# Optimization experiments

Measured on AMD Instinct MI355X. Metric: run time of the kernel, lower is better.

Reference implementation:

```python
import jax, jax.numpy as jnp
import numpy as np

NX, NY = 512, 512
FNUM, GNUM = 120, 120
NA = 1.35
WAVELENGTH = NX * NA / 100.0  # chosen so normalized period = 100
N_LIQUID = 1.44
M_RED = 0.25
LOW_LIGHT_THRES = 1e-3
SRC_STEEP = 8.0
RESIST_STEEP = 30.0
RESIST_INT = 0.225
DOSES = (0.98, 1.0, 1.02)
SRC_GRID = 13

X1 = NX // 2 - FNUM; X2 = NX // 2 + FNUM + 1
Y1 = NY // 2 - GNUM; Y2 = NY // 2 + GNUM + 1
_PER_X = NX / (WAVELENGTH / NA)
_PER_Y = NY / (WAVELENGTH / NA)
NORM_SPEC = _PER_X * _PER_Y
DFMDG = 1.0 / NORM_SPEC
_fm = (np.arange(X1, X2) - NX // 2) / _PER_X
_gm = (np.arange(Y1, Y2) - NY // 2) / _PER_Y
_FM, _GM = np.meshgrid(_fm, _gm)  # 'xy' indexing, shape [2*GNUM+1, 2*FNUM+1]
FM = jnp.asarray(_FM, jnp.float32)
GM = jnp.asarray(_GM, jnp.float32)


def cal_pupil(fg2):
    # obliquity factor; pupil phase is identically zero in this module
    num = 1.0 - (M_RED ** 2) * (NA ** 2) * fg2
    den = 1.0 - (NA / N_LIQUID) ** 2 * fg2
    return jnp.sqrt(jnp.sqrt(num / den))


def setup_inputs() -> dict:
    key = jax.random.key(0)
    g = np.linspace(-1.0, 1.0, SRC_GRID, dtype=np.float32)
    fxg, fyg = np.meshgrid(g, g)
    r = np.sqrt(fxg ** 2 + fyg ** 2)
    data = ((r >= 0.6) & (r <= 0.9)).astype(np.float32)  # annular source
    # sigmoid activation init: +1 where lit, -1 elsewhere (zeros, set 2 where data>0.5, sub 1)
    params = 2.0 * data - 1.0
    mask_value = jax.random.uniform(key, (NY, NX), jnp.float32)
    return {
        "mask_value": mask_value,
        "source_params": jnp.asarray(params, jnp.float32),
        "source_fx": jnp.asarray(fxg.reshape(-1), jnp.float32),
        "source_fy": jnp.asarray(fyg.reshape(-1), jnp.float32),
    }


def _forward(mask_value, source_params, source_fx, source_fy):
    # source activation + low-light pruning (masked_select expressed as zero-weighting)
    val = jax.nn.sigmoid(SRC_STEEP * source_params).reshape(-1)  # [S]
    valid = val >= LOW_LIGHT_THRES
    w = jnp.where(valid, val, 0.0)
    weight = jnp.sum(w)

    # normalization intensity (detached in the original)
    fxy2 = source_fx ** 2 + source_fy ** 2
    obl = cal_pupil(jnp.where(valid, fxy2, 0.0))
    norm_I = jax.lax.stop_gradient(
        N_LIQUID * DFMDG ** 2 * jnp.sum(w * (NORM_SPEC * obl) ** 2) / weight
    )

    # shifted pupil per source point over the mask frequency window
    F = FM[None, :, :] + source_fx[:, None, None]  # [S, Gy, Gx]
    G = GM[None, :, :] + source_fy[:, None, None]
    rho2 = F * F + G * G                            # == mask_fg2m + 2(fx*fm+fy*gm) + fxy2
    vmask = rho2 <= 1.0
    pupil = jnp.where(vmask, cal_pupil(jnp.where(vmask, rho2, 0.0)), 0.0)  # [S, Gy, Gx]

    S = w.shape[0]
    Is, Rs = [], []
    for d in DOSES:
        fv = jnp.fft.fftshift(jnp.fft.fft2(jnp.fft.ifftshift(mask_value * d)))
        win = fv[Y1:Y2, X1:X2]                      # [Gy, Gx] complex
        tempH = win[None, :, :] * pupil.astype(jnp.complex64)  # masked spectrum*pupil
        e = jnp.zeros((S, NY, NX), jnp.complex64).at[:, Y1:Y2, X1:X2].set(tempH)
        AA = jnp.fft.fftshift(jnp.fft.ifft2(e), axes=(-2, -1))
        I2 = AA.real ** 2 + AA.imag ** 2            # |AA * conj(AA)|
        intensity = jnp.einsum('s,syx->yx', w, I2) / weight / norm_I
        Is.append(intensity)
        Rs.append(jax.nn.sigmoid(RESIST_STEEP * (intensity - RESIST_INT)))
    # [2, 3, NY, NX]: [0] = aerial intensity per dose, [1] = resist image per dose
    return jnp.stack([jnp.stack(Is), jnp.stack(Rs)])


def reference(mask_value, source_params, source_fx, source_fy):
    return _forward(mask_value, source_params, source_fx, source_fy)
```

## Files before the change

### kernel.cpp

```cpp
#include <hip/hip_runtime.h>
#include <hip/hip_bf16.h>
#include <hip/hip_fp16.h>


#define SPLIT 8

static const size_t O_ACC  = 8192;
static const size_t ACC_BYTES = (size_t)SPLIT * 512 * 512 * 4;
static const size_t O_WIN  = O_ACC + ACC_BYTES;
static const size_t O_R1   = O_WIN + 464896;
static const size_t O_T2   = O_R1 + 987136;
static const size_t SLOT_BYTES = (size_t)512 * 244 * 4;

__device__ inline float2 cadd(float2 a, float2 b){ return make_float2(a.x+b.x, a.y+b.y); }
__device__ inline float2 csub(float2 a, float2 b){ return make_float2(a.x-b.x, a.y-b.y); }
__device__ inline float2 cmul(float2 a, float2 b){
  return make_float2(fmaf(a.x, b.x, -(a.y*b.y)), fmaf(a.x, b.y, a.y*b.x));
}
__device__ inline float2 twsgn(float2 t, int S) {
  return make_float2(t.x, (S > 0) ? t.y : -t.y);
}

__device__ inline void build_twt(float2* twt) {
  for (int k = (int)threadIdx.x; k < 512; k += 256) {
    double a = 6.283185307179586476925286766559 * (double)k / 512.0;
    twt[k] = make_float2((float)cos(a), (float)sin(a));
  }
}

template<int S, bool ZTOP>
__device__ inline void dft8(float2 v[8]) {
  const float sg = (float)S;
  const float C7 = 0.7071067811865476f;
  float2 t0, t1, t2, t3, t4, t5, t6, t7;
  if (ZTOP) {
    t0 = v[0]; t4 = v[0];
    t1 = v[1]; t5 = v[1];
    t2 = v[2]; t6 = v[2];
    t3 = v[3]; t7 = v[3];
  } else {
    t0=cadd(v[0],v[4]); t4=csub(v[0],v[4]);
    t1=cadd(v[1],v[5]); t5=csub(v[1],v[5]);
    t2=cadd(v[2],v[6]); t6=csub(v[2],v[6]);
    t3=cadd(v[3],v[7]); t7=csub(v[3],v[7]);
  }
  t5 = make_float2(C7*(t5.x - sg*t5.y), C7*(t5.y + sg*t5.x));
  t6 = make_float2(-sg*t6.y, sg*t6.x);
  t7 = make_float2(C7*(-t7.x - sg*t7.y), C7*(sg*t7.x - t7.y));
  float2 u0=cadd(t0,t2), u2=csub(t0,t2);
  float2 u1=cadd(t1,t3), u3=csub(t1,t3);
  u3 = make_float2(-sg*u3.y, sg*u3.x);
  float2 u4=cadd(t4,t6), u6=csub(t4,t6);
  float2 u5=cadd(t5,t7), u7=csub(t5,t7);
  u7 = make_float2(-sg*u7.y, sg*u7.x);
  v[0]=cadd(u0,u1); v[4]=csub(u0,u1);
  v[2]=cadd(u2,u3); v[6]=csub(u2,u3);
  v[1]=cadd(u4,u5); v[5]=csub(u4,u5);
  v[3]=cadd(u6,u7); v[7]=csub(u6,u7);
}

template<int S, bool ZTOP>
__device__ inline void wfft512(float2 v[8], int lane, float2* xch,
                               const float2* twt) {
  const int p2 = lane & 7, u0 = lane >> 3;
  dft8<S, ZTOP>(v);
  { float2 t1 = twsgn(twt[lane], S), acc = t1;
    v[1] = cmul(v[1], acc);
    #pragma unroll
    for (int u = 2; u < 8; u++) { acc = cmul(acc, t1); v[u] = cmul(v[u], acc); } }
  __builtin_amdgcn_wave_barrier();
  #pragma unroll
  for (int u = 0; u < 8; u++) xch[u*68 + p2*8 + u0] = v[u];
  __builtin_amdgcn_wave_barrier();
  { const float4* rp = (const float4*)(xch + u0*68 + p2*8);
    #pragma unroll
    for (int q = 0; q < 4; q++) {
      float4 t = rp[q];
      v[2*q]   = make_float2(t.x, t.y);
      v[2*q+1] = make_float2(t.z, t.w);
    } }
  dft8<S, false>(v);
  { float2 t1 = twsgn(twt[p2 << 3], S), acc = t1;
    v[1] = cmul(v[1], acc);
    #pragma unroll
    for (int u = 2; u < 8; u++) { acc = cmul(acc, t1); v[u] = cmul(v[u], acc); } }
  __builtin_amdgcn_wave_barrier();
  #pragma unroll
  for (int u = 0; u < 8; u++) xch[u*68 + lane] = v[u];
  __builtin_amdgcn_wave_barrier();
  { const float4* rp = (const float4*)(xch + p2*68 + u0*8);
    #pragma unroll
    for (int q = 0; q < 4; q++) {
      float4 t = rp[q];
      v[2*q]   = make_float2(t.x, t.y);
      v[2*q+1] = make_float2(t.z, t.w);
    } }
  dft8<S, false>(v);
}

__global__ void __launch_bounds__(256, 6) k_b1(const float* mask, const float* prm,
                                               const float* sfx, const float* sfy,
                                               char* ws, float2* R1t) {
  int t = threadIdx.x, lane = t & 63, wv = t >> 6;
  __shared__ __align__(16) float2 lds[4*544];
  __shared__ __align__(16) float2 twt[512];
  build_twt(twt);
  if (blockIdx.x == 0) {
    float*  sw  = (float*)lds;
    float*  sxx = sw + 192; float* syy = sxx + 192; float* scw = syy + 192;
    double* so  = (double*)(sw + 768);
    int*    skp = (int*)(so + 176);
    if (t < 169) {
      float p = prm[t];
      float val = 1.f / (1.f + __expf(-8.f * p));
      float w = (val >= 0.001f) ? val : 0.f;
      double o = 0.0; float fx = 0.f, fy = 0.f;
      if (w > 0.f) {
        fx = sfx[t]; fy = sfy[t];
        double f2 = (double)fx*(double)fx + (double)fy*(double)fy;
        o = (double)w * sqrt((1.0 - 0.11390625 * f2) / (1.0 - 0.87890625 * f2));
      }
      sw[t] = w; so[t] = o; sxx[t] = fx; syy[t] = fy;
    }
    __syncthreads();
    if (t < 169) {
      float w = sw[t];
      int keep = 0; float cw = w;
      if (w > 0.f) {
        float fx = sxx[t], fy = syy[t];
        int pr = -1;
        for (int s2 = 0; s2 < 169; s2++) {
          if (sw[s2] > 0.f && fabsf(sxx[s2] + fx) < 1e-5f
                           && fabsf(syy[s2] + fy) < 1e-5f) { pr = s2; break; }
        }
        if (pr < 0 || pr == t) keep = 1;
        else if (pr > t) { keep = 1; cw = w + sw[pr]; }
      }
      skp[t] = keep; scw[t] = cw;
    }
    __syncthreads();
    if (t == 0) {
      float* wsf = (float*)ws;
      double Sden = 0.0; int c = 0;
      for (int s = 0; s < 169; s++) {
        Sden += so[s];
        if (skp[s]) { wsf[64+c] = scw[s]; wsf[320+c] = sxx[s]; wsf[576+c] = syy[s]; c++; }
      }
      ((int*)ws)[0] = c;
      wsf[1] = (float)(1.0 / (262144.0 * 1.44 * Sden));
    }
  }
  __syncthreads();
  int y = blockIdx.x * 4 + wv;
  float2 v[8];
  #pragma unroll
  for (int q = 0; q < 8; q++) v[q] = make_float2(mask[y*512 + 64*q + lane], 0.f);
  wfft512<-1, false>(v, lane, lds + wv*544, twt);
  #pragma unroll
  for (int u = 0; u < 8; u++) {
    int k = (lane>>3) + 8*(lane&7) + 64*u;
    int beta = (k >= 392) ? (k - 392) : ((k <= 120) ? (k + 120) : -1);
    if (beta >= 0) R1t[beta*512 + y] = v[u];
  }
}

__global__ void __launch_bounds__(256, 6) k_b2(const float2* R1t, float2* Wg) {
  int lane = threadIdx.x & 63, wv = threadIdx.x >> 6;
  int j = blockIdx.x * 4 + wv;
  __shared__ __align__(16) float2 lds[4*544];
  __shared__ __align__(16) float2 twt[512];
  build_twt(twt);
  __syncthreads();
  float2 v[8];
  #pragma unroll
  for (int q = 0; q < 8; q++)
    v[q] = (j < 241) ? R1t[j*512 + 64*q + lane] : make_float2(0.f, 0.f);
  wfft512<-1, false>(v, lane, lds + wv*544, twt);
  if (j < 241) {
    #pragma unroll
    for (int u = 0; u < 8; u++) {
      int k = (lane>>3) + 8*(lane&7) + 64*u;
      int alpha = (k >= 392) ? (k - 392) : ((k <= 120) ? (k + 120) : -1);
      if (alpha >= 0) Wg[alpha*241 + j] = v[u];
    }
  }
}

__global__ void __launch_bounds__(256, 7) k_c1(const float2* Wg, const char* wsb,
                                               int base, int CH, __half2* T2) {
  const float* wsf = (const float*)wsb;
  __shared__ __align__(16) float2 lds[4*544];
  __shared__ __align__(16) float2 twt[512];
  __shared__ float FMt[241];
  build_twt(twt);
  if (threadIdx.x < 241)
    FMt[threadIdx.x] = (float)(((double)((int)threadIdx.x - 120)) / 100.0);
  __syncthreads();
  int active = *(const int*)wsb - base;
  if (active > CH) active = CH;
  int ntask = active * 31;
  int lane = threadIdx.x & 63, wv = threadIdx.x >> 6;
  float2* xch = lds + wv*544;
  for (int task = (int)blockIdx.x; task < ntask; task += (int)gridDim.x) {
    int sic  = task / 31;
    int tile = task % 31;
    int slot = base + sic;
    float fx = wsf[320 + slot], fy = wsf[576 + slot];
    float sqw = __fsqrt_rn(wsf[64 + slot]) * 0.001953125f;
    #pragma unroll
    for (int ph = 0; ph < 2; ph++) {
      int alpha = tile*8 + ph*4 + wv;
      bool arow = (alpha < 241);
      float Gf = __fadd_rn(arow ? FMt[alpha] : 0.f, fy);
      float g2 = __fmul_rn(Gf, Gf);
      bool active_row = arow && (g2 <= 1.0f);
      float2 v[8];
      #pragma unroll
      for (int q = 0; q < 8; q++) v[q] = make_float2(0.f, 0.f);
      if (active_row) {
        #pragma unroll
        for (int q = 0; q < 4; q++) {
          int n = 64*q + lane;
          if (n < 241) {
            float Ff = __fadd_rn(FMt[n], fx);
            float r2 = __fadd_rn(__fmul_rn(Ff, Ff), g2);
            if (r2 <= 1.0f) {
              float num = fmaf(-0.11390625f, r2, 1.0f);
              float den = fmaf(-0.87890625f, r2, 1.0f);
              float P = __fsqrt_rn(__fsqrt_rn(__fdividef(num, den))) * sqw;
              float2 Wv = Wg[alpha*241 + n];
              v[q] = make_float2(P * Wv.x, P * Wv.y);
            }
          }
        }
        wfft512<1, true>(v, lane, xch, twt);
      }
      #pragma unroll
      for (int u = 0; u < 8; u++) {
        int xx = (lane>>3) + 8*(lane&7) + 64*u;
        xch[xx] = v[u];
      }
      __syncthreads();
      int colb = tile*8 + ph*4;
      if (colb < 244) {
        #pragma unroll
        for (int r = 0; r < 2; r++) {
          int x = (int)threadIdx.x + 256*r;
          union { __half2 h[4]; float4 f; } u;
          #pragma unroll
          for (int wvi = 0; wvi < 4; wvi++) {
            float2 a = lds[wvi*544 + x];
            u.h[wvi] = __floats2half2_rn(a.x, a.y);
          }
          *(float4*)(T2 + ((size_t)sic*512 + x)*244 + colb) = u.f;
        }
      }
      __syncthreads();
    }
  }
}

__global__ void __launch_bounds__(256, 7) k_c2(const __half2* T2, const char* wsb,
                                               int base, int CH, int first,
                                               float* accbuf) {
  const int* cnt = (const int*)wsb;
  int part = blockIdx.x & (SPLIT-1);
  int xg   = blockIdx.x >> 3;
  int lane = threadIdx.x & 63, wv = threadIdx.x >> 6;
  int x = xg*4 + wv;
  __shared__ __align__(16) float2 lds[4*544];
  __shared__ __align__(16) float2 twt[512];
  build_twt(twt);
  __syncthreads();
  float2* xch = lds + wv*544;
  int count = *cnt;
  float av[8] = {0.f,0.f,0.f,0.f,0.f,0.f,0.f,0.f};
  int sic = part;
  bool act = (sic < CH) && (base + sic < count);
  __half2 pv[4] = {{0.f,0.f},{0.f,0.f},{0.f,0.f},{0.f,0.f}};
  if (act) {
    const __half2* row = T2 + ((size_t)sic*512 + x)*244;
    #pragma unroll
    for (int q = 0; q < 4; q++) {
      int n = 64*q + lane;
      pv[q] = (n < 241) ? row[n] : __half2{0.f, 0.f};
    }
  }
  while (act) {
    float2 v[8];
    #pragma unroll
    for (int q = 0; q < 4; q++) { float2 f = __half22float2(pv[q]); v[q] = f; }
    #pragma unroll
    for (int q = 4; q < 8; q++) v[q] = make_float2(0.f, 0.f);
    int nsic = sic + SPLIT;
    act = (nsic < CH) && (base + nsic < count);
    if (act) {
      const __half2* row = T2 + ((size_t)nsic*512 + x)*244;
      #pragma unroll
      for (int q = 0; q < 4; q++) {
        int n = 64*q + lane;
        pv[q] = (n < 241) ? row[n] : __half2{0.f, 0.f};
      }
    }
    wfft512<1, true>(v, lane, xch, twt);
    #pragma unroll
    for (int u = 0; u < 8; u++)
      av[u] += fmaf(v[u].x, v[u].x, v[u].y*v[u].y);
    sic = nsic;
  }
  float* a = accbuf + ((size_t)part << 18) + (size_t)x * 512;
  int y0 = (lane>>3) + 8*(lane&7);
  if (first) {
    #pragma unroll
    for (int u = 0; u < 8; u++) a[y0 + 64*u] = av[u];
  } else {
    #pragma unroll
    for (int u = 0; u < 8; u++) a[y0 + 64*u] += av[u];
  }
}

__global__ void __launch_bounds__(256) k_final(const float* acc, const char* wsb,
                                               float* out) {
  __shared__ float tile[64][65];
  const float* wsf = (const float*)wsb;
  float scale = wsf[1];
  int x0 = (blockIdx.x & 7) * 64, y0 = (blockIdx.x >> 3) * 64;
  int j = threadIdx.x & 63, i0 = threadIdx.x >> 6;
  #pragma unroll
  for (int k = 0; k < 16; k++) {
    int i = i0 + 4*k;
    const float* ap = acc + (size_t)(x0 + i)*512 + y0 + j;
    float s = 0.f;
    #pragma unroll
    for (int p = 0; p < SPLIT; p++) s += ap[(size_t)p << 18];
    tile[i][j] = s;
  }
  __syncthreads();
  const float dd[3] = {0.9604f, 1.0f, 1.0404f};
  #pragma unroll
  for (int k = 0; k < 16; k++) {
    int yy = i0 + 4*k;
    float I = scale * tile[j][yy];
    int o = (y0 + yy)*512 + x0 + j;
    #pragma unroll
    for (int d = 0; d < 3; d++) {
      float Ik = dd[d] * I;
      out[(size_t)d*262144 + o] = Ik;
      out[(size_t)(3+d)*262144 + o] = 1.f / (1.f + __expf(-30.f*(Ik - 0.225f)));
    }
  }
}

extern "C" void kernel_launch(void* const* d_in, const int* in_sizes, int n_in,
                              void* d_out, int out_size, void* d_ws, size_t ws_size,
                              hipStream_t stream) {
  (void)in_sizes; (void)n_in; (void)out_size;
  const float* mask = (const float*)d_in[0];
  const float* prm  = (const float*)d_in[1];
  const float* sfx  = (const float*)d_in[2];
  const float* sfy  = (const float*)d_in[3];
  float* out = (float*)d_out;
  char*  ws  = (char*)d_ws;

  float*   acc = (float*)(ws + O_ACC);
  float2*  Wg  = (float2*)(ws + O_WIN);
  float2*  R1t = (float2*)(ws + O_R1);
  __half2* T2  = (__half2*)(ws + O_T2);

  k_b1<<<dim3(128), dim3(256), 0, stream>>>(mask, prm, sfx, sfy, ws, R1t);
  k_b2<<<dim3(61),  dim3(256), 0, stream>>>(R1t, Wg);

  size_t avail = (ws_size > O_T2) ? (ws_size - O_T2) : 0;
  int CH = (int)(avail / SLOT_BYTES);
  if (CH > 169) CH = 169;
  if (CH < 1)   CH = 1;
  for (int base = 0; base < 169; base += CH) {
    k_c1<<<dim3(1024),      dim3(256), 0, stream>>>(Wg, (const char*)ws, base, CH, T2);
    k_c2<<<dim3(128*SPLIT), dim3(256), 0, stream>>>(T2, (const char*)ws, base, CH,
                                                    (base == 0) ? 1 : 0, acc);
  }
  k_final<<<dim3(64), dim3(256), 0, stream>>>(acc, (const char*)ws, out);
}
```

Baseline: 138.2 us.

## Fuse column FFT accumulation with final epilogue when all sources fit workspace

```diff
diff --git a/kernel.cpp b/kernel.cpp
--- a/kernel.cpp
+++ b/kernel.cpp
@@ -260,6 +260,74 @@
   }
 }
 
+__global__ void __launch_bounds__(256, 7) k_c2ep(const __half2* T2, const char* wsb,
+                                                 float* out) {
+  const float* wsf = (const float*)wsb;
+  int count = *(const int*)wsb;
+  float scale = wsf[1];
+  int x = blockIdx.x;
+  int t = threadIdx.x, lane = t & 63, wv = t >> 6;
+  __shared__ __align__(16) float2 lds[4*544];
+  __shared__ __align__(16) float2 twt[512];
+  build_twt(twt);
+  __syncthreads();
+  float2* xch = lds + wv*544;
+  float av[8] = {0.f,0.f,0.f,0.f,0.f,0.f,0.f,0.f};
+  int sic = wv;
+  bool act = (sic < count);
+  __half2 pv[4] = {{0.f,0.f},{0.f,0.f},{0.f,0.f},{0.f,0.f}};
+  if (act) {
+    const __half2* row = T2 + ((size_t)sic*512 + x)*244;
+    #pragma unroll
+    for (int q = 0; q < 4; q++) {
+      int n = 64*q + lane;
+      pv[q] = (n < 241) ? row[n] : __half2{0.f, 0.f};
+    }
+  }
+  while (act) {
+    float2 v[8];
+    #pragma unroll
+    for (int q = 0; q < 4; q++) { float2 f = __half22float2(pv[q]); v[q] = f; }
+    #pragma unroll
+    for (int q = 4; q < 8; q++) v[q] = make_float2(0.f, 0.f);
+    int nsic = sic + 4;
+    act = (nsic < count);
+    if (act) {
+      const __half2* row = T2 + ((size_t)nsic*512 + x)*244;
+      #pragma unroll
+      for (int q = 0; q < 4; q++) {
+        int n = 64*q + lane;
+        pv[q] = (n < 241) ? row[n] : __half2{0.f, 0.f};
+      }
+    }
+    wfft512<1, true>(v, lane, xch, twt);
+    #pragma unroll
+    for (int u = 0; u < 8; u++)
+      av[u] += fmaf(v[u].x, v[u].x, v[u].y*v[u].y);
+    sic = nsic;
+  }
+  __syncthreads();
+  float* buf = (float*)lds;
+  int y0 = (lane>>3) + 8*(lane&7);
+  #pragma unroll
+  for (int u = 0; u < 8; u++) buf[wv*512 + y0 + 64*u] = av[u];
+  __syncthreads();
+  const float dd[3] = {0.9604f, 1.0f, 1.0404f};
+  #pragma unroll
+  for (int r = 0; r < 2; r++) {
+    int y = t + 256*r;
+    float s = buf[y] + buf[512 + y] + buf[1024 + y] + buf[1536 + y];
+    float I = scale * s;
+    int o = y*512 + x;
+    #pragma unroll
+    for (int d = 0; d < 3; d++) {
+      float Ik = dd[d] * I;
+      out[(size_t)d*262144 + o] = Ik;
+      out[(size_t)(3+d)*262144 + o] = 1.f / (1.f + __expf(-30.f*(Ik - 0.225f)));
+    }
+  }
+}
+
 __global__ void __launch_bounds__(256, 7) k_c2(const __half2* T2, const char* wsb,
                                                int base, int CH, int first,
                                                float* accbuf) {
@@ -374,10 +442,15 @@
   int CH = (int)(avail / SLOT_BYTES);
   if (CH > 169) CH = 169;
   if (CH < 1)   CH = 1;
-  for (int base = 0; base < 169; base += CH) {
-    k_c1<<<dim3(1024),      dim3(256), 0, stream>>>(Wg, (const char*)ws, base, CH, T2);
-    k_c2<<<dim3(128*SPLIT), dim3(256), 0, stream>>>(T2, (const char*)ws, base, CH,
-                                                    (base == 0) ? 1 : 0, acc);
-  }
-  k_final<<<dim3(64), dim3(256), 0, stream>>>(acc, (const char*)ws, out);
-}
+  if (CH >= 169) {
+    k_c1 <<<dim3(1024), dim3(256), 0, stream>>>(Wg, (const char*)ws, 0, 169, T2);
+    k_c2ep<<<dim3(512), dim3(256), 0, stream>>>(T2, (const char*)ws, out);
+  } else {
+    for (int base = 0; base < 169; base += CH) {
+      k_c1<<<dim3(1024),      dim3(256), 0, stream>>>(Wg, (const char*)ws, base, CH, T2);
+      k_c2<<<dim3(128*SPLIT), dim3(256), 0, stream>>>(T2, (const char*)ws, base, CH,
+                                                      (base == 0) ? 1 : 0, acc);
+    }
+    k_final<<<dim3(64), dim3(256), 0, stream>>>(acc, (const char*)ws, out);
+  }
+}
```

Result: no change. 139.1 us (+0.6%).
